# Optimization experiments

Measured on AMD Instinct MI355X. Metric: run time of the kernel, lower is better.

Reference implementation:

```python
import jax, jax.numpy as jnp
import numpy as np

B, T, X, DC, DW, H = 64, 512, 8, 128, 128, 128
NEG = 1e20  # mask constant from the original '-1e20 trick'


def setup_inputs() -> dict:
    key = jax.random.key(0)
    ks = jax.random.split(key, 8)
    inp = jax.random.normal(ks[0], (B, T, DC), dtype=jnp.float32)
    skip_words = jax.random.normal(ks[1], (B, T, X, DW), dtype=jnp.float32)
    rng = np.random.default_rng(0)
    # skip edge source s at position t indexes history slot s+1, which must be <= t -> s <= t-1
    src = rng.integers(0, T, size=(B, T, X))
    src = np.minimum(src, np.maximum(np.arange(T) - 1, 0)[None, :, None]).astype(np.int32)
    cnt = np.minimum(rng.integers(0, X + 1, size=(B, T)), np.arange(T)[None, :]).astype(np.int32)
    s = 0.1
    return {
        'inp': inp,
        'skip_words': skip_words,
        'seq_len': jnp.full((B,), T, dtype=jnp.int32),
        'skip_sources': jnp.asarray(src),
        'skip_count': jnp.asarray(cnt),
        'w_ih_c': jax.random.normal(ks[2], (DC, 3 * H), dtype=jnp.float32) * s,
        'w_hh_c': jax.random.normal(ks[3], (H, 3 * H), dtype=jnp.float32) * s,
        'bias_c': jnp.zeros((3 * H,), dtype=jnp.float32),
        'a_ih': jax.random.normal(ks[4], (DC, H), dtype=jnp.float32) * s,
        'a_hh': jax.random.normal(ks[5], (H, H), dtype=jnp.float32) * s,
        'a_bias': jnp.zeros((H,), dtype=jnp.float32),
        'w_ih_w': jax.random.normal(ks[6], (DW, 3 * H), dtype=jnp.float32) * s,
        'w_hh_w': jax.random.normal(ks[7], (H, 3 * H), dtype=jnp.float32) * s,
        'bias_w': jnp.zeros((3 * H,), dtype=jnp.float32),
    }


def _forward(inp, skip_words, w_ih_c, w_hh_c, bias_c, a_ih, a_hh, a_bias,
             w_ih_w, w_hh_w, bias_w, skip_sources, skip_count):
    Bv, Tv, Xv, _ = skip_words.shape
    Hh = w_hh_c.shape[0]
    # Precompute all input projections (time-independent) outside the scan.
    wi_c_all = jnp.einsum('btd,dk->btk', inp, w_ih_c) + bias_c          # [B,T,3H]
    a_wi_all = jnp.einsum('btd,dh->bth', inp, a_ih) + a_bias            # [B,T,H]
    wi_w_all = jnp.einsum('btxd,dk->btxk', skip_words, w_ih_w) + bias_w  # [B,T,X,3H]
    iota = jnp.arange(Xv)

    def step(carry, xs):
        h_hist, c_hist = carry  # [B, T+1, H] states; slot t+1 written at step t
        t, wi_c, wi_w, a_wi, src, cnt = xs
        h0 = jnp.take(h_hist, t, axis=1)                                 # [B,H]
        idx = (src + 1)[:, :, None]                                      # skip_before_head=False
        c_x = jnp.take_along_axis(c_hist, idx, axis=1)                   # [B,X,H]
        h_x = jnp.take_along_axis(h_hist, idx, axis=1)                   # [B,X,H]
        # WordLSTMCell: c1 = sig(f)*c_x + sig(i)*tanh(g)
        gw = jnp.einsum('bxh,hk->bxk', h_x, w_hh_w) + wi_w               # [B,X,3H]
        f_w, i_w, g_w = jnp.split(gw, 3, axis=-1)
        c1_skip = jax.nn.sigmoid(f_w) * c_x + jax.nn.sigmoid(i_w) * jnp.tanh(g_w)
        # MultiInputLSTMCell: gated merge over {g} U skip cells
        gc = h0 @ w_hh_c + wi_c                                          # [B,3H]
        i_g, o_g, g_g = jnp.split(gc, 3, axis=-1)
        i_g = jax.nn.sigmoid(i_g)[:, None]                               # [B,1,H]
        o_g = jax.nn.sigmoid(o_g)                                        # [B,H]
        g_g = jnp.tanh(g_g)[:, None]                                     # [B,1,H]
        alpha = jax.nn.sigmoid(a_wi[:, None] + jnp.einsum('bxh,hk->bxk', c1_skip, a_hh))
        mask = (iota[None, :] >= cnt[:, None]).astype(alpha.dtype)[:, :, None] * NEG
        ealpha = jnp.exp(jnp.concatenate([i_g, alpha - mask], axis=1))   # [B,1+X,H]
        alpha_n = ealpha / ealpha.sum(axis=1, keepdims=True)
        merged = jnp.concatenate([g_g, c1_skip], axis=1)                 # [B,1+X,H]
        c1 = (merged * alpha_n).sum(axis=1)                              # [B,H]
        h1 = o_g * jnp.tanh(c1)
        h_hist = jax.lax.dynamic_update_slice(h_hist, h1[:, None], (0, t + 1, 0))
        c_hist = jax.lax.dynamic_update_slice(c_hist, c1[:, None], (0, t + 1, 0))
        return (h_hist, c_hist), (h1, c1)

    init = (jnp.zeros((Bv, Tv + 1, Hh), inp.dtype), jnp.zeros((Bv, Tv + 1, Hh), inp.dtype))
    xs = (jnp.arange(Tv), wi_c_all.swapaxes(0, 1), wi_w_all.swapaxes(0, 1),
          a_wi_all.swapaxes(0, 1), skip_sources.swapaxes(0, 1), skip_count.swapaxes(0, 1))
    _, (hs, cs) = jax.lax.scan(step, init, xs)
    return hs.swapaxes(0, 1), cs.swapaxes(0, 1)  # [B,T,H] each


def reference(inp, skip_words, w_ih_c, w_hh_c, bias_c, a_ih, a_hh, a_bias,
              w_ih_w, w_hh_w, bias_w, seq_len, skip_sources, skip_count):
    # seq_len only determines max_seq_len in the torch code; here T is static = inp.shape[1]
    return _forward(inp, skip_words, w_ih_c, w_hh_c, bias_c, a_ih, a_hh, a_bias,
                    w_ih_w, w_hh_w, bias_w, skip_sources, skip_count)
```

## Files before the change

kernel.cpp:

```cpp
#include <hip/hip_runtime.h>

typedef unsigned short u16;
typedef unsigned int u32;
typedef __attribute__((ext_vector_type(8))) short short8;
typedef __attribute__((ext_vector_type(4))) float f32x4;

constexpr int CB = 64, CT = 512, CX = 8, CH = 128;

__device__ __forceinline__ u16 f2b(float f) {
  u32 u = __float_as_uint(f);
  return (u16)((u + 0x7FFFu + ((u >> 16) & 1u)) >> 16);
}
__device__ __forceinline__ u32 pack2bf(float2 v) {
  return (u32)f2b(v.x) | ((u32)f2b(v.y) << 16);
}
__device__ __forceinline__ float sigf(float x) {
  return __fdividef(1.0f, 1.0f + __expf(-x));
}
__device__ __forceinline__ float tanhfast(float x) {
  return 1.0f - __fdividef(2.0f, __expf(2.0f * x) + 1.0f);
}
__device__ __forceinline__ f32x4 mfma16(short8 a, short8 b, f32x4 c) {
  return __builtin_amdgcn_mfma_f32_16x16x32_bf16(a, b, c, 0, 0, 0);
}
__device__ __forceinline__ int aswz(int row, int k) {
  return row * 256 + ((k & 0xC0) | ((((k >> 3) ^ row) & 7) << 3) | (k & 7));
}
__device__ __forceinline__ int pswz(int row, int k) {
  return row * 128 + ((k & 0x40) | ((((k >> 3) ^ (row & 7)) & 7) << 3) | (k & 7));
}


__global__ void prep_kernel(const float* __restrict__ w_ih_c, const float* __restrict__ w_hh_c,
                            const float* __restrict__ a_ih, const float* __restrict__ a_hh,
                            const float* __restrict__ w_ih_w, const float* __restrict__ w_hh_w,
                            u16* __restrict__ WgwT, u16* __restrict__ WahcT, u16* __restrict__ WcaT) {
  int gid = blockIdx.x * blockDim.x + threadIdx.x;
  if (gid < 98304) {
    int n = gid >> 8, k = gid & 255;
    float v = (k < 128) ? w_hh_w[k * 384 + n] : w_ih_w[(k - 128) * 384 + n];
    WgwT[gid] = f2b(v);
  } else if (gid < 163840) {
    int i = gid - 98304; int n = i >> 7, k = i & 127;
    float v = (n < 128) ? a_hh[k * 128 + n] : w_hh_c[k * 384 + (n - 128)];
    WahcT[i] = f2b(v);
  } else if (gid < 229376) {
    int i = gid - 163840; int n = i >> 7, k = i & 127;
    float v = (n < 384) ? w_ih_c[k * 384 + n] : a_ih[k * 128 + (n - 384)];
    WcaT[i] = f2b(v);
  }
}

__global__ __launch_bounds__(256) void proj_kernel(const float* __restrict__ inp,
    const u16* __restrict__ WcaT, const float* __restrict__ bias_c,
    const float* __restrict__ a_bias, float* __restrict__ wica) {
  const int m0 = blockIdx.x * 64;
  const int wv = threadIdx.x >> 6, ln = threadIdx.x & 63;
  const int l16 = ln & 15, qd = ln >> 4;
  const int arow = m0 + wv * 16 + l16;
  short8 af[4];
#pragma unroll
  for (int kt = 0; kt < 4; ++kt) {
    const float* p = inp + (size_t)arow * 128 + kt * 32 + qd * 8;
    float4 x0 = *(const float4*)p;
    float4 x1 = *(const float4*)(p + 4);
    short8 a;
    a[0] = (short)f2b(x0.x); a[1] = (short)f2b(x0.y); a[2] = (short)f2b(x0.z); a[3] = (short)f2b(x0.w);
    a[4] = (short)f2b(x1.x); a[5] = (short)f2b(x1.y); a[6] = (short)f2b(x1.z); a[7] = (short)f2b(x1.w);
    af[kt] = a;
  }
  for (int nt = 0; nt < 32; ++nt) {
    const int col = nt * 16 + l16;
    f32x4 acc = {0.f, 0.f, 0.f, 0.f};
#pragma unroll
    for (int kt = 0; kt < 4; ++kt) {
      short8 bf = *(const short8*)(WcaT + (size_t)col * 128 + kt * 32 + qd * 8);
      acc = mfma16(af[kt], bf, acc);
    }
    const float bias = (col < 384) ? bias_c[col] : a_bias[col - 384];
#pragma unroll
    for (int r = 0; r < 4; ++r) {
      const int orow = m0 + wv * 16 + qd * 4 + r;
      wica[(size_t)orow * 512 + col] = acc[r] + bias;
    }
  }
}

__global__ __launch_bounds__(512) void scan_kernel(
    const float* __restrict__ skip_words,
    const int* __restrict__ srcp,
    const int* __restrict__ cntp,
    const float* __restrict__ bias_w,
    const u16* __restrict__ WgwT,
    const u16* __restrict__ WahcT,
    const float* __restrict__ wica,
    float* __restrict__ out)
{
  const int b = blockIdx.x;
  const int tid = threadIdx.x;
  const int wv = tid >> 6, ln = tid & 63, l16 = ln & 15, qd = ln >> 4;
  const int h = wv * 16 + l16;

  float* hs = out + (size_t)b * CT * CH;
  float* cs = out + (size_t)(CB + b) * CT * CH;
  const float* swb = skip_words + (size_t)b * CT * CX * CH;
  const int* srb = srcp + b * CT * CX;
  const int* cnb = cntp + b * CT;
  const float* wicab = wica + (size_t)b * CT * 512;

  __shared__ __align__(16) u16 Asg[16 * 256];
  __shared__ __align__(16) u16 Psg[16 * 128];
  __shared__ __align__(16) u16 Gsg[16 * 128];
  __shared__ __align__(16) float Csg[16 * 132];
  __shared__ __align__(16) u32 pad_occ[15360];
  if ((int)blockIdx.x < 0) pad_occ[tid] = tid;

  for (int i = tid; i < 2048; i += 512) ((u32*)Asg)[i] = 0;
  for (int i = tid; i < 1024; i += 512) ((u32*)Psg)[i] = 0;
  for (int i = tid; i < 1024; i += 512) ((u32*)Gsg)[i] = 0;

  short8 wgwf[3][8];
#pragma unroll
  for (int g = 0; g < 3; ++g) {
    const int n = g * 128 + h;
#pragma unroll
    for (int kt = 0; kt < 8; ++kt)
      wgwf[g][kt] = *(const short8*)(WgwT + (size_t)n * 256 + kt * 32 + qd * 8);
  }
  short8 waca[4];
#pragma unroll
  for (int kt = 0; kt < 4; ++kt)
    waca[kt] = *(const short8*)(WahcT + (size_t)h * 128 + kt * 32 + qd * 8);
  short8 wacc[3][4];
#pragma unroll
  for (int g = 0; g < 3; ++g) {
    const int n = 128 + g * 128 + h;
#pragma unroll
    for (int kt = 0; kt < 4; ++kt)
      wacc[g][kt] = *(const short8*)(WahcT + (size_t)n * 128 + kt * 32 + qd * 8);
  }
  const float bw0 = bias_w[h], bw1 = bias_w[128 + h], bw2 = bias_w[256 + h];

  __syncthreads();

  {
    const int s0 = srb[wv];
    float2 hA = *(const float2*)(hs + (size_t)s0 * CH + 2 * ln);
    float2 cA = *(const float2*)(cs + (size_t)s0 * CH + 2 * ln);
    float2 wA = *(const float2*)(swb + (size_t)wv * CH + 2 * ln);
    *(u32*)&Asg[aswz(wv, 2 * ln)] = pack2bf(hA);
    *(u32*)&Asg[aswz(wv, 128 + 2 * ln)] = pack2bf(wA);
    *(float2*)&Csg[wv * 132 + 2 * ln] = cA;
  }
  int srcF = srb[CX + wv];
  __syncthreads();

  for (int t = 0; t < CT; ++t) {
    const int cntc = cnb[t];
    const float wi0 = wicab[(size_t)t * 512 + h];
    const float wi1 = wicab[(size_t)t * 512 + 128 + h];
    const float wi2 = wicab[(size_t)t * 512 + 256 + h];
    const float wi3 = wicab[(size_t)t * 512 + 384 + h];
    const bool st = (t + 1 < CT);
    bool fr = false;
    float2 hA = {0.f, 0.f}, cA = {0.f, 0.f}, wA = {0.f, 0.f};
    int fm = 0, srcFn = 0;
    if (st) {
      fr = (srcF == t);
      if (!fr) {
        hA = *(const float2*)(hs + (size_t)srcF * CH + 2 * ln);
        cA = *(const float2*)(cs + (size_t)srcF * CH + 2 * ln);
      }
      wA = *(const float2*)(swb + ((size_t)(t + 1) * CX + wv) * CH + 2 * ln);
      int4 a0 = *(const int4*)(srb + (t + 1) * CX);
      int4 a1 = *(const int4*)(srb + (t + 1) * CX + 4);
      fm = (a0.x == t) | ((a0.y == t) << 1) | ((a0.z == t) << 2) | ((a0.w == t) << 3) |
           ((a1.x == t) << 4) | ((a1.y == t) << 5) | ((a1.z == t) << 6) | ((a1.w == t) << 7);
      if (t + 2 < CT) srcFn = srb[(t + 2) * CX + wv];
    }

    f32x4 d0 = {0.f, 0.f, 0.f, 0.f}, d1 = d0, d2 = d0;
    f32x4 e1 = d0, e2 = d0, e3 = d0;
#pragma unroll
    for (int kt = 0; kt < 8; ++kt) {
      short8 a = *(const short8*)&Asg[aswz(l16, kt * 32 + qd * 8)];
      d0 = mfma16(a, wgwf[0][kt], d0);
      d1 = mfma16(a, wgwf[1][kt], d1);
      d2 = mfma16(a, wgwf[2][kt], d2);
    }
#pragma unroll
    for (int kt = 0; kt < 4; ++kt) {
      short8 g = *(const short8*)&Gsg[pswz(l16, kt * 32 + qd * 8)];
      e1 = mfma16(g, wacc[0][kt], e1);
      e2 = mfma16(g, wacc[1][kt], e2);
      e3 = mfma16(g, wacc[2][kt], e3);
    }
    float c1s[4] = {0.f, 0.f, 0.f, 0.f};
    if (qd < 2) {
#pragma unroll
      for (int r = 0; r < 4; ++r) {
        const int row = qd * 4 + r;
        const float cx = Csg[row * 132 + h];
        const float v = sigf(d0[r] + bw0) * cx + sigf(d1[r] + bw1) * tanhfast(d2[r] + bw2);
        c1s[r] = v;
        Psg[pswz(row, h)] = f2b(v);
      }
    }
    asm volatile("s_waitcnt lgkmcnt(0)\n\ts_barrier" ::: "memory");

    f32x4 e0 = {0.f, 0.f, 0.f, 0.f};
#pragma unroll
    for (int kt = 0; kt < 4; ++kt) {
      short8 p = *(const short8*)&Psg[pswz(l16, kt * 32 + qd * 8)];
      e0 = mfma16(p, waca[kt], e0);
    }

    const float gi = __shfl(e1[0], l16, 64);
    const float go = __shfl(e2[0], l16, 64);
    const float gg = __shfl(e3[0], l16, 64);
    const float i_g = sigf(gi + wi0);
    const float o_g = sigf(go + wi1);
    const float g_g = tanhfast(gg + wi2);
    float pe = 0.f, pec = 0.f;
#pragma unroll
    for (int r = 0; r < 4; ++r) {
      const int row = qd * 4 + r;
      if (row < cntc) {
        const float e = __expf(sigf(e0[r] + wi3));
        pe += e;
        pec += e * c1s[r];
      }
    }
    pe += __shfl_xor(pe, 16, 64);  pec += __shfl_xor(pec, 16, 64);
    pe += __shfl_xor(pe, 32, 64);  pec += __shfl_xor(pec, 32, 64);
    const float ei = __expf(i_g);
    const float c1 = __fdividef(ei * g_g + pec, ei + pe);
    const float h1 = o_g * tanhfast(c1);

    if (qd == 0) {
      hs[(size_t)t * CH + h] = h1;
      cs[(size_t)t * CH + h] = c1;
      Gsg[pswz(0, h)] = f2b(h1);
      if (fm) {
        const u16 hb = f2b(h1);
#pragma unroll
        for (int s = 0; s < 8; ++s)
          if ((fm >> s) & 1) {
            Asg[aswz(s, h)] = hb;
            Csg[s * 132 + h] = c1;
          }
      }
    }
    if (st) {
      if (!fr) {
        *(u32*)&Asg[aswz(wv, 2 * ln)] = pack2bf(hA);
        *(float2*)&Csg[wv * 132 + 2 * ln] = cA;
      }
      *(u32*)&Asg[aswz(wv, 128 + 2 * ln)] = pack2bf(wA);
    }
    __syncthreads();
    srcF = srcFn;
  }
}

extern "C" void kernel_launch(void* const* d_in, const int* in_sizes, int n_in,
                              void* d_out, int out_size, void* d_ws, size_t ws_size,
                              hipStream_t stream) {
  (void)in_sizes; (void)n_in; (void)out_size; (void)ws_size;
  const float* inp    = (const float*)d_in[0];
  const float* skw    = (const float*)d_in[1];
  const int*   ssrc   = (const int*)d_in[3];
  const int*   scnt   = (const int*)d_in[4];
  const float* w_ih_c = (const float*)d_in[5];
  const float* w_hh_c = (const float*)d_in[6];
  const float* bias_c = (const float*)d_in[7];
  const float* a_ih   = (const float*)d_in[8];
  const float* a_hh   = (const float*)d_in[9];
  const float* a_bias = (const float*)d_in[10];
  const float* w_ih_w = (const float*)d_in[11];
  const float* w_hh_w = (const float*)d_in[12];
  const float* bias_w = (const float*)d_in[13];

  char* ws = (char*)d_ws;
  u16*   WgwT  = (u16*)(ws);
  u16*   WahcT = (u16*)(ws + 196608);
  u16*   WcaT  = (u16*)(ws + 327680);
  float* wica  = (float*)(ws + 458752);
  float* out   = (float*)d_out;

  prep_kernel<<<224, 1024, 0, stream>>>(w_ih_c, w_hh_c, a_ih, a_hh, w_ih_w, w_hh_w,
                                        WgwT, WahcT, WcaT);
  proj_kernel<<<512, 256, 0, stream>>>(inp, WcaT, bias_c, a_bias, wica);
  scan_kernel<<<64, 512, 0, stream>>>(skw, ssrc, scnt, bias_w, WgwT, WahcT, wica, out);
}
```

Baseline: 1.570 ms.

## Precompute swizzled LDS pointers, change P swizzle, drop occupancy padding

Hoists all LDS swizzle address computations out of the time loop into per-thread base pointers, and changes the P/G swizzle to XOR with row>>1 to cut bank conflicts on the P stores. It removes the large shared padding array that limited occupancy and replaces launch_bounds with explicit flat-work-group and waves-per-eu attributes. The softmax mask becomes branchless. These cut per-step integer work on the serial scan's critical path, but the new attributes can change register allocation.

New measurement: 1.532 ms. -2.4%, faster.

```diff
diff --git a/kernel.cpp b/kernel.cpp
--- a/kernel.cpp
+++ b/kernel.cpp
@@ -23,11 +23,13 @@
 __device__ __forceinline__ f32x4 mfma16(short8 a, short8 b, f32x4 c) {
   return __builtin_amdgcn_mfma_f32_16x16x32_bf16(a, b, c, 0, 0, 0);
 }
-__device__ __forceinline__ int aswz(int row, int k) {
-  return row * 256 + ((k & 0xC0) | ((((k >> 3) ^ row) & 7) << 3) | (k & 7));
-}
-__device__ __forceinline__ int pswz(int row, int k) {
-  return row * 128 + ((k & 0x40) | ((((k >> 3) ^ (row & 7)) & 7) << 3) | (k & 7));
+__device__ __forceinline__ int aswz2(int row, int k) {
+  int c = k >> 3;
+  return row * 256 + ((c >> 3) * 64) + (((c & 7) ^ (row & 7)) * 8) + (k & 7);
+}
+__device__ __forceinline__ int pswz2(int row, int k) {
+  int c = k >> 3;
+  return row * 128 + ((c >> 3) * 64) + (((c & 7) ^ ((row >> 1) & 7)) * 8) + (k & 7);
 }
 
 
@@ -86,7 +88,8 @@
   }
 }
 
-__global__ __launch_bounds__(512) void scan_kernel(
+__global__ __attribute__((amdgpu_flat_work_group_size(512, 512), amdgpu_waves_per_eu(1, 2)))
+void scan_kernel(
     const float* __restrict__ skip_words,
     const int* __restrict__ srcp,
     const int* __restrict__ cntp,
@@ -112,12 +115,23 @@
   __shared__ __align__(16) u16 Psg[16 * 128];
   __shared__ __align__(16) u16 Gsg[16 * 128];
   __shared__ __align__(16) float Csg[16 * 132];
-  __shared__ __align__(16) u32 pad_occ[15360];
-  if ((int)blockIdx.x < 0) pad_occ[tid] = tid;
 
   for (int i = tid; i < 2048; i += 512) ((u32*)Asg)[i] = 0;
   for (int i = tid; i < 1024; i += 512) ((u32*)Psg)[i] = 0;
   for (int i = tid; i < 1024; i += 512) ((u32*)Gsg)[i] = 0;
+
+  const u16* aRe = Asg + l16 * 256 + ((qd ^ (l16 & 7)) * 8);
+  const u16* aRo = Asg + l16 * 256 + (((qd | 4) ^ (l16 & 7)) * 8);
+  const u16* pRe = Psg + l16 * 128 + ((qd ^ ((l16 >> 1) & 7)) * 8);
+  const u16* pRo = Psg + l16 * 128 + (((qd | 4) ^ ((l16 >> 1) & 7)) * 8);
+  const u16* gRe = Gsg + l16 * 128 + ((qd ^ ((l16 >> 1) & 7)) * 8);
+  const u16* gRo = Gsg + l16 * 128 + (((qd | 4) ^ ((l16 >> 1) & 7)) * 8);
+  u16* aW = Asg + wv * 256 + (ln >> 5) * 64 + ((((ln >> 2) & 7) ^ (wv & 7)) * 8) + ((2 * ln) & 7);
+  u16* pW01 = Psg + (qd * 4) * 128 + (h >> 6) * 64 + ((((h >> 3) & 7) ^ (2 * qd)) * 8) + (h & 7);
+  u16* pW23 = Psg + (qd * 4 + 2) * 128 + (h >> 6) * 64 + ((((h >> 3) & 7) ^ (2 * qd + 1)) * 8) + (h & 7);
+  u16* gW = Gsg + (h >> 6) * 64 + (((h >> 3) & 7) * 8) + (h & 7);
+  const float* cR = Csg + (qd * 4) * 132 + h;
+  float* cW = Csg + wv * 132 + 2 * ln;
 
   short8 wgwf[3][8];
 #pragma unroll
@@ -148,19 +162,17 @@
     float2 hA = *(const float2*)(hs + (size_t)s0 * CH + 2 * ln);
     float2 cA = *(const float2*)(cs + (size_t)s0 * CH + 2 * ln);
     float2 wA = *(const float2*)(swb + (size_t)wv * CH + 2 * ln);
-    *(u32*)&Asg[aswz(wv, 2 * ln)] = pack2bf(hA);
-    *(u32*)&Asg[aswz(wv, 128 + 2 * ln)] = pack2bf(wA);
-    *(float2*)&Csg[wv * 132 + 2 * ln] = cA;
+    *(u32*)aW = pack2bf(hA);
+    *(u32*)(aW + 128) = pack2bf(wA);
+    *(float2*)cW = cA;
   }
   int srcF = srb[CX + wv];
   __syncthreads();
 
   for (int t = 0; t < CT; ++t) {
     const int cntc = cnb[t];
-    const float wi0 = wicab[(size_t)t * 512 + h];
-    const float wi1 = wicab[(size_t)t * 512 + 128 + h];
-    const float wi2 = wicab[(size_t)t * 512 + 256 + h];
-    const float wi3 = wicab[(size_t)t * 512 + 384 + h];
+    const float* wp = wicab + (size_t)t * 512 + h;
+    const float wi0 = wp[0], wi1 = wp[128], wi2 = wp[256], wi3 = wp[384];
     const bool st = (t + 1 < CT);
     bool fr = false;
     float2 hA = {0.f, 0.f}, cA = {0.f, 0.f}, wA = {0.f, 0.f};
@@ -183,14 +195,14 @@
     f32x4 e1 = d0, e2 = d0, e3 = d0;
 #pragma unroll
     for (int kt = 0; kt < 8; ++kt) {
-      short8 a = *(const short8*)&Asg[aswz(l16, kt * 32 + qd * 8)];
+      short8 a = *(const short8*)((kt & 1 ? aRo : aRe) + (kt >> 1) * 64);
       d0 = mfma16(a, wgwf[0][kt], d0);
       d1 = mfma16(a, wgwf[1][kt], d1);
       d2 = mfma16(a, wgwf[2][kt], d2);
     }
 #pragma unroll
     for (int kt = 0; kt < 4; ++kt) {
-      short8 g = *(const short8*)&Gsg[pswz(l16, kt * 32 + qd * 8)];
+      short8 g = *(const short8*)((kt & 1 ? gRo : gRe) + (kt >> 1) * 64);
       e1 = mfma16(g, wacc[0][kt], e1);
       e2 = mfma16(g, wacc[1][kt], e2);
       e3 = mfma16(g, wacc[2][kt], e3);
@@ -199,11 +211,11 @@
     if (qd < 2) {
 #pragma unroll
       for (int r = 0; r < 4; ++r) {
-        const int row = qd * 4 + r;
-        const float cx = Csg[row * 132 + h];
+        const float cx = cR[r * 132];
         const float v = sigf(d0[r] + bw0) * cx + sigf(d1[r] + bw1) * tanhfast(d2[r] + bw2);
         c1s[r] = v;
-        Psg[pswz(row, h)] = f2b(v);
+        u16* pw = (r < 2 ? pW01 : pW23);
+        pw[(r & 1) * 128] = f2b(v);
       }
     }
     asm volatile("s_waitcnt lgkmcnt(0)\n\ts_barrier" ::: "memory");
@@ -211,7 +223,7 @@
     f32x4 e0 = {0.f, 0.f, 0.f, 0.f};
 #pragma unroll
     for (int kt = 0; kt < 4; ++kt) {
-      short8 p = *(const short8*)&Psg[pswz(l16, kt * 32 + qd * 8)];
+      short8 p = *(const short8*)((kt & 1 ? pRo : pRe) + (kt >> 1) * 64);
       e0 = mfma16(p, waca[kt], e0);
     }
 
@@ -225,11 +237,10 @@
 #pragma unroll
     for (int r = 0; r < 4; ++r) {
       const int row = qd * 4 + r;
-      if (row < cntc) {
-        const float e = __expf(sigf(e0[r] + wi3));
-        pe += e;
-        pec += e * c1s[r];
-      }
+      const float e = __expf(sigf(e0[r] + wi3));
+      const bool ok = (row < cntc);
+      pe += ok ? e : 0.f;
+      pec += ok ? e * c1s[r] : 0.f;
     }
     pe += __shfl_xor(pe, 16, 64);  pec += __shfl_xor(pec, 16, 64);
     pe += __shfl_xor(pe, 32, 64);  pec += __shfl_xor(pec, 32, 64);
@@ -240,23 +251,23 @@
     if (qd == 0) {
       hs[(size_t)t * CH + h] = h1;
       cs[(size_t)t * CH + h] = c1;
-      Gsg[pswz(0, h)] = f2b(h1);
+      *gW = f2b(h1);
       if (fm) {
         const u16 hb = f2b(h1);
 #pragma unroll
         for (int s = 0; s < 8; ++s)
           if ((fm >> s) & 1) {
-            Asg[aswz(s, h)] = hb;
+            Asg[aswz2(s, h)] = hb;
             Csg[s * 132 + h] = c1;
           }
       }
     }
     if (st) {
       if (!fr) {
-        *(u32*)&Asg[aswz(wv, 2 * ln)] = pack2bf(hA);
-        *(float2*)&Csg[wv * 132 + 2 * ln] = cA;
+        *(u32*)aW = pack2bf(hA);
+        *(float2*)cW = cA;
       }
-      *(u32*)&Asg[aswz(wv, 128 + 2 * ln)] = pack2bf(wA);
+      *(u32*)(aW + 128) = pack2bf(wA);
     }
     __syncthreads();
     srcF = srcFn;
```
